# Optimization experiments

Measured on AMD Instinct MI355X. Metric: run time of the kernel, lower is better.

Reference implementation:

```python
import jax, jax.numpy as jnp
import numpy as np

NUM_EMBEDDINGS = 1024
EMBEDDING_DIM = 128
COMMITMENT_COST = 0.25


def setup_inputs() -> dict:
    key = jax.random.key(0)
    k1, k2 = jax.random.split(key)
    z = jax.random.normal(k1, (16, EMBEDDING_DIM, 64, 64), dtype=jnp.float32)
    # codebook initialized uniform(-1/K, 1/K) as in the torch module
    codebook = jax.random.uniform(
        k2, (NUM_EMBEDDINGS, EMBEDDING_DIM), dtype=jnp.float32,
        minval=-1.0 / NUM_EMBEDDINGS, maxval=1.0 / NUM_EMBEDDINGS)
    return {"z": z, "codebook": codebook}


def reference(z, codebook):
    B, C = z.shape[0], z.shape[1]
    K = codebook.shape[0]
    # (B, C, H, W) -> (B*H*W, C)
    z_flat = z.reshape(B, C, -1).transpose(0, 2, 1).reshape(-1, C)
    N = z_flat.shape[0]

    # squared L2 distances (same argmin as cdist p=2)
    d2 = (jnp.sum(z_flat * z_flat, axis=1, keepdims=True)
          - 2.0 * (z_flat @ codebook.T)
          + jnp.sum(codebook * codebook, axis=1))  # [N, K]
    indices = jnp.argmin(d2, axis=1)               # [N]

    quantized_flat = codebook[indices]             # [N, C] gather
    q_raw = quantized_flat.reshape(B, -1, C).transpose(0, 2, 1).reshape(z.shape)

    # training-mode losses (F.mse_loss = mean squared error)
    commitment_loss = jnp.mean((z - jax.lax.stop_gradient(q_raw)) ** 2)
    codebook_loss = jnp.mean((q_raw - jax.lax.stop_gradient(z)) ** 2)
    vq_loss = codebook_loss + COMMITMENT_COST * commitment_loss

    # straight-through estimator
    quantized = z + jax.lax.stop_gradient(q_raw - z)

    # perplexity over code usage (zero-count codes contribute 0 to entropy)
    counts = jax.ops.segment_sum(jnp.ones((N,), jnp.float32), indices,
                                 num_segments=K)
    probs = counts / jnp.float32(N)
    perplexity = jnp.exp(-jnp.sum(probs * jnp.log(probs + 1e-10)))

    return quantized, indices, vq_loss, perplexity
```

## Files before the change

### kernel.cpp

```cpp
#include <hip/hip_runtime.h>
#include <math.h>

namespace {
constexpr int CDIM   = 128;
constexpr int KCODES = 1024;
constexpr int HWSZ   = 4096;
constexpr int BATCH  = 16;
constexpr int NPOS   = BATCH * HWSZ;
constexpr int P      = 128;
constexpr int TK     = 128;
constexpr int NTILES = KCODES / TK;
constexpr int THREADS = 512;
constexpr size_t QELEMS   = (size_t)BATCH * CDIM * HWSZ;
constexpr size_t IDX_OFF  = QELEMS;
constexpr size_t LOSS_OFF = IDX_OFF + (size_t)NPOS;
constexpr size_t PERP_OFF = LOSS_OFF + 1;
constexpr int WS_C2   = 0;
constexpr int WS_HIST = 1024;
constexpr int WS_LOSS = 2048;
constexpr float INV_TOTAL = 1.0f / (float)QELEMS;
constexpr float INV_NPOS  = 1.0f / (float)NPOS;
}

__device__ __forceinline__ float np_sumsq_128(const float* v) {
    float r[8];
    #pragma unroll
    for (int j = 0; j < 8; ++j) r[j] = __fmul_rn(v[j], v[j]);
    #pragma unroll
    for (int i = 8; i < 128; i += 8) {
        #pragma unroll
        for (int j = 0; j < 8; ++j)
            r[j] = __fadd_rn(r[j], __fmul_rn(v[i + j], v[i + j]));
    }
    const float s01 = __fadd_rn(r[0], r[1]);
    const float s23 = __fadd_rn(r[2], r[3]);
    const float s45 = __fadd_rn(r[4], r[5]);
    const float s67 = __fadd_rn(r[6], r[7]);
    return __fadd_rn(__fadd_rn(s01, s23), __fadd_rn(s45, s67));
}

__global__ __launch_bounds__(256) void vq_prep(const float* __restrict__ cb,
                                               float* __restrict__ ws) {
    const int k = blockIdx.x * 256 + threadIdx.x;
    const float* row = cb + (size_t)k * CDIM;
    float rr[CDIM];
    #pragma unroll
    for (int c = 0; c < CDIM; ++c) rr[c] = row[c];
    ws[WS_C2 + k] = np_sumsq_128(rr);
    ((unsigned int*)ws)[WS_HIST + k] = 0u;
    if (k == 0) ws[WS_LOSS] = 0.0f;
}

__global__ __launch_bounds__(512, 1) void vq_main(const float* __restrict__ z,
                                                  const float* __restrict__ cb,
                                                  float* __restrict__ ws,
                                                  float* __restrict__ out) {
    __shared__ __align__(16) float zt[CDIM][P];
    __shared__ __align__(16) float tile[TK * CDIM];
    __shared__ float z2s[P];
    __shared__ float bdls[16][P];
    __shared__ int   bkls[16][P];
    __shared__ int   wkls[P];
    __shared__ float red[THREADS];

    const int tid   = threadIdx.x;
    const int nbase = blockIdx.x * P;
    const int b     = nbase >> 12;
    const int hw0   = nbase & (HWSZ - 1);
    const float* zb = z + (size_t)b * CDIM * HWSZ + hw0;

    #pragma unroll
    for (int i = 0; i < (CDIM * P / 4) / THREADS; ++i) {
        const int linear = i * THREADS + tid;
        const int c  = linear >> 5;
        const int p4 = (linear & 31) * 4;
        *(float4*)&zt[c][p4] = *(const float4*)(zb + (size_t)c * HWSZ + p4);
    }
    {
        const float4* src = (const float4*)cb;
        float4* w4 = (float4*)tile;
        #pragma unroll
        for (int i = 0; i < (TK * CDIM / 4) / THREADS; ++i) {
            const int idx = i * THREADS + tid;
            const int k = idx >> 5;
            const int f = idx & 31;
            w4[(k << 5) | (f ^ ((k >> 3) & 3))] = src[idx];
        }
    }
    __syncthreads();

    if (tid < P) {
        const int p = tid;
        float r[8];
        #pragma unroll
        for (int j = 0; j < 8; ++j) {
            const float x = zt[j][p];
            r[j] = __fmul_rn(x, x);
        }
        #pragma unroll
        for (int i = 8; i < CDIM; i += 8) {
            #pragma unroll
            for (int j = 0; j < 8; ++j) {
                const float x = zt[i + j][p];
                r[j] = __fadd_rn(r[j], __fmul_rn(x, x));
            }
        }
        const float s01 = __fadd_rn(r[0], r[1]);
        const float s23 = __fadd_rn(r[2], r[3]);
        const float s45 = __fadd_rn(r[4], r[5]);
        const float s67 = __fadd_rn(r[6], r[7]);
        z2s[p] = __fadd_rn(__fadd_rn(s01, s23), __fadd_rn(s45, s67));
    }
    __syncthreads();

    const int pg  = tid & 31;
    const int cg  = tid >> 5;
    const int p0  = pg * 4;
    const int k0  = cg * 8;
    const int scg = cg & 3;
    const float* c2g = ws + WS_C2;

    float z2r[4];
    #pragma unroll
    for (int i = 0; i < 4; ++i) z2r[i] = z2s[p0 + i];

    float bestd[4] = {INFINITY, INFINITY, INFINITY, INFINITY};
    int   bestk[4] = {0, 0, 0, 0};

    const float4* t4 = (const float4*)tile;

    for (int t = 0; t < NTILES; ++t) {
        float a[4][8];
        #pragma unroll
        for (int i = 0; i < 4; ++i)
            #pragma unroll
            for (int j = 0; j < 8; ++j) a[i][j] = 0.0f;

        #pragma unroll 2
        for (int c4 = 0; c4 < CDIM / 4; ++c4) {
            const int c = c4 * 4;
            const float4 zv0 = *(const float4*)&zt[c + 0][p0];
            const float4 zv1 = *(const float4*)&zt[c + 1][p0];
            const float4 zv2 = *(const float4*)&zt[c + 2][p0];
            const float4 zv3 = *(const float4*)&zt[c + 3][p0];
            const int col = c4 ^ scg;
            float4 cv[8];
            #pragma unroll
            for (int j = 0; j < 8; ++j) cv[j] = t4[((k0 + j) << 5) | col];
            #pragma unroll
            for (int j = 0; j < 8; ++j) {
                a[0][j] = fmaf(zv0.x, cv[j].x, a[0][j]);
                a[0][j] = fmaf(zv1.x, cv[j].y, a[0][j]);
                a[0][j] = fmaf(zv2.x, cv[j].z, a[0][j]);
                a[0][j] = fmaf(zv3.x, cv[j].w, a[0][j]);
                a[1][j] = fmaf(zv0.y, cv[j].x, a[1][j]);
                a[1][j] = fmaf(zv1.y, cv[j].y, a[1][j]);
                a[1][j] = fmaf(zv2.y, cv[j].z, a[1][j]);
                a[1][j] = fmaf(zv3.y, cv[j].w, a[1][j]);
                a[2][j] = fmaf(zv0.z, cv[j].x, a[2][j]);
                a[2][j] = fmaf(zv1.z, cv[j].y, a[2][j]);
                a[2][j] = fmaf(zv2.z, cv[j].z, a[2][j]);
                a[2][j] = fmaf(zv3.z, cv[j].w, a[2][j]);
                a[3][j] = fmaf(zv0.w, cv[j].x, a[3][j]);
                a[3][j] = fmaf(zv1.w, cv[j].y, a[3][j]);
                a[3][j] = fmaf(zv2.w, cv[j].z, a[3][j]);
                a[3][j] = fmaf(zv3.w, cv[j].w, a[3][j]);
            }
        }

        const int kb = t * TK + k0;
        #pragma unroll
        for (int j = 0; j < 8; ++j) {
            const float c2 = c2g[kb + j];
            #pragma unroll
            for (int i = 0; i < 4; ++i) {
                const float d = __fadd_rn(fmaf(-2.0f, a[i][j], z2r[i]), c2);
                if (d < bestd[i]) { bestd[i] = d; bestk[i] = kb + j; }
            }
        }

        if (t + 1 < NTILES) {
            __syncthreads();
            const float4* src = (const float4*)(cb + (size_t)(t + 1) * TK * CDIM);
            float4* w4 = (float4*)tile;
            #pragma unroll
            for (int i = 0; i < (TK * CDIM / 4) / THREADS; ++i) {
                const int idx = i * THREADS + tid;
                const int k = idx >> 5;
                const int f = idx & 31;
                w4[(k << 5) | (f ^ ((k >> 3) & 3))] = src[idx];
            }
            __syncthreads();
        }
    }

    #pragma unroll
    for (int i = 0; i < 4; ++i) {
        bdls[cg][p0 + i] = bestd[i];
        bkls[cg][p0 + i] = bestk[i];
    }
    __syncthreads();

    unsigned int* ghist = (unsigned int*)ws + WS_HIST;
    if (tid < P) {
        const int p = tid;
        float bd = bdls[0][p];
        int   bk = bkls[0][p];
        #pragma unroll
        for (int g = 1; g < 16; ++g) {
            const float d = bdls[g][p];
            const int   k = bkls[g][p];
            if (d < bd || (d == bd && k < bk)) { bd = d; bk = k; }
        }
        wkls[p] = bk;
        out[IDX_OFF + (size_t)(nbase + p)] = (float)bk;
        atomicAdd(&ghist[bk], 1u);
        red[tid] = bd;
    } else {
        red[tid] = 0.0f;
    }
    __syncthreads();
    for (int s = THREADS / 2; s > 0; s >>= 1) {
        if (tid < s) red[tid] += red[tid + s];
        __syncthreads();
    }
    if (tid == 0) atomicAdd(&ws[WS_LOSS], red[0]);

    float* ob = out + (size_t)b * CDIM * HWSZ + hw0;
    #pragma unroll
    for (int i = 0; i < (CDIM * P) / THREADS; ++i) {
        const int linear = i * THREADS + tid;
        const int c = linear >> 7;
        const int p = linear & 127;
        ob[(size_t)c * HWSZ + p] = cb[(size_t)wkls[p] * CDIM + c];
    }
}

__global__ __launch_bounds__(1024) void vq_final(const float* __restrict__ ws,
                                                 float* __restrict__ out) {
    __shared__ float red[1024];
    const int t = threadIdx.x;
    const unsigned int* hist = (const unsigned int*)ws + WS_HIST;
    const float p = (float)hist[t] * INV_NPOS;
    red[t] = p * logf(p + 1e-10f);
    __syncthreads();
    for (int s = 512; s > 0; s >>= 1) {
        if (t < s) red[t] += red[t + s];
        __syncthreads();
    }
    if (t == 0) {
        out[LOSS_OFF] = 1.25f * (ws[WS_LOSS] * INV_TOTAL);
        out[PERP_OFF] = expf(-red[0]);
    }
}

extern "C" void kernel_launch(void* const* d_in, const int* in_sizes, int n_in,
                              void* d_out, int out_size, void* d_ws, size_t ws_size,
                              hipStream_t stream) {
    const float* z  = (const float*)d_in[0];
    const float* cb = (const float*)d_in[1];
    float* out = (float*)d_out;
    float* ws  = (float*)d_ws;

    vq_prep <<<KCODES / 256, 256, 0, stream>>>(cb, ws);
    vq_main <<<NPOS / P,     THREADS, 0, stream>>>(z, cb, ws, out);
    vq_final<<<1,           1024, 0, stream>>>(ws, out);
}
```

Measured before the change: 313.3 us.

## Read codebook directly from global memory and raise occupancy target

Drops the shared-memory codebook tile and its per-tile barriers. Each thread now loads its codebook rows straight from global memory through the cache, and the launch-bounds occupancy hint rises from 1 to 4 blocks. The cross-group argmin now pairs groups with a wave shuffle, halving the shared-memory partials. In exchange the inner loop depends on global-load latency, and the occupancy hint caps registers for a loop that already holds 32 accumulators plus 32 codebook values, so spilling is likely. The 64 KB z tile per block also limits how many blocks fit in LDS anyway.

```diff
diff --git a/kernel.cpp b/kernel.cpp
--- a/kernel.cpp
+++ b/kernel.cpp
@@ -51,15 +51,14 @@
     if (k == 0) ws[WS_LOSS] = 0.0f;
 }
 
-__global__ __launch_bounds__(512, 1) void vq_main(const float* __restrict__ z,
+__global__ __launch_bounds__(512, 4) void vq_main(const float* __restrict__ z,
                                                   const float* __restrict__ cb,
                                                   float* __restrict__ ws,
                                                   float* __restrict__ out) {
     __shared__ __align__(16) float zt[CDIM][P];
-    __shared__ __align__(16) float tile[TK * CDIM];
     __shared__ float z2s[P];
-    __shared__ float bdls[16][P];
-    __shared__ int   bkls[16][P];
+    __shared__ float bdls[8][P];
+    __shared__ int   bkls[8][P];
     __shared__ int   wkls[P];
     __shared__ float red[THREADS];
 
@@ -76,17 +75,6 @@
         const int p4 = (linear & 31) * 4;
         *(float4*)&zt[c][p4] = *(const float4*)(zb + (size_t)c * HWSZ + p4);
     }
-    {
-        const float4* src = (const float4*)cb;
-        float4* w4 = (float4*)tile;
-        #pragma unroll
-        for (int i = 0; i < (TK * CDIM / 4) / THREADS; ++i) {
-            const int idx = i * THREADS + tid;
-            const int k = idx >> 5;
-            const int f = idx & 31;
-            w4[(k << 5) | (f ^ ((k >> 3) & 3))] = src[idx];
-        }
-    }
     __syncthreads();
 
     if (tid < P) {
@@ -113,12 +101,12 @@
     }
     __syncthreads();
 
-    const int pg  = tid & 31;
-    const int cg  = tid >> 5;
-    const int p0  = pg * 4;
-    const int k0  = cg * 8;
-    const int scg = cg & 3;
+    const int pg = tid & 31;
+    const int cg = tid >> 5;
+    const int p0 = pg * 4;
+    const int k0 = cg * 8;
     const float* c2g = ws + WS_C2;
+    const float4* cb4 = (const float4*)cb;
 
     float z2r[4];
     #pragma unroll
@@ -127,26 +115,25 @@
     float bestd[4] = {INFINITY, INFINITY, INFINITY, INFINITY};
     int   bestk[4] = {0, 0, 0, 0};
 
-    const float4* t4 = (const float4*)tile;
-
     for (int t = 0; t < NTILES; ++t) {
+        const int kb = t * TK + k0;
+        const float4* crow = cb4 + (size_t)kb * 32;
+
         float a[4][8];
         #pragma unroll
         for (int i = 0; i < 4; ++i)
             #pragma unroll
             for (int j = 0; j < 8; ++j) a[i][j] = 0.0f;
 
-        #pragma unroll 2
         for (int c4 = 0; c4 < CDIM / 4; ++c4) {
             const int c = c4 * 4;
             const float4 zv0 = *(const float4*)&zt[c + 0][p0];
             const float4 zv1 = *(const float4*)&zt[c + 1][p0];
             const float4 zv2 = *(const float4*)&zt[c + 2][p0];
             const float4 zv3 = *(const float4*)&zt[c + 3][p0];
-            const int col = c4 ^ scg;
             float4 cv[8];
             #pragma unroll
-            for (int j = 0; j < 8; ++j) cv[j] = t4[((k0 + j) << 5) | col];
+            for (int j = 0; j < 8; ++j) cv[j] = crow[(size_t)j * 32 + c4];
             #pragma unroll
             for (int j = 0; j < 8; ++j) {
                 a[0][j] = fmaf(zv0.x, cv[j].x, a[0][j]);
@@ -168,7 +155,6 @@
             }
         }
 
-        const int kb = t * TK + k0;
         #pragma unroll
         for (int j = 0; j < 8; ++j) {
             const float c2 = c2g[kb + j];
@@ -178,26 +164,22 @@
                 if (d < bestd[i]) { bestd[i] = d; bestk[i] = kb + j; }
             }
         }
-
-        if (t + 1 < NTILES) {
-            __syncthreads();
-            const float4* src = (const float4*)(cb + (size_t)(t + 1) * TK * CDIM);
-            float4* w4 = (float4*)tile;
-            #pragma unroll
-            for (int i = 0; i < (TK * CDIM / 4) / THREADS; ++i) {
-                const int idx = i * THREADS + tid;
-                const int k = idx >> 5;
-                const int f = idx & 31;
-                w4[(k << 5) | (f ^ ((k >> 3) & 3))] = src[idx];
-            }
-            __syncthreads();
-        }
     }
 
     #pragma unroll
     for (int i = 0; i < 4; ++i) {
-        bdls[cg][p0 + i] = bestd[i];
-        bkls[cg][p0 + i] = bestk[i];
+        const float od = __shfl_xor(bestd[i], 32);
+        const int   ok = __shfl_xor(bestk[i], 32);
+        if (od < bestd[i] || (od == bestd[i] && ok < bestk[i])) {
+            bestd[i] = od; bestk[i] = ok;
+        }
+    }
+    if ((tid & 32) == 0) {
+        #pragma unroll
+        for (int i = 0; i < 4; ++i) {
+            bdls[cg >> 1][p0 + i] = bestd[i];
+            bkls[cg >> 1][p0 + i] = bestk[i];
+        }
     }
     __syncthreads();
 
@@ -207,7 +189,7 @@
         float bd = bdls[0][p];
         int   bk = bkls[0][p];
         #pragma unroll
-        for (int g = 1; g < 16; ++g) {
+        for (int g = 1; g < 8; ++g) {
             const float d = bdls[g][p];
             const int   k = bkls[g][p];
             if (d < bd || (d == bd && k < bk)) { bd = d; bk = k; }
```

Result: slower. 348.2 us (+11.1%).
